# Optimization experiments

Hardware: AMD Instinct MI355X
Metric: run time of the kernel (lower is better)

Reference implementation:

```python
import jax, jax.numpy as jnp
import numpy as np

B, S, HID = 4, 2048, 2048
NH, NKV = 8, 1
HD = HID // NH  # 256
G = NH // NKV   # queries per kv head
ROPE_THETA = 10000.0
NEG_INF = -1e9


def setup_inputs() -> dict:
    key = jax.random.key(0)
    ks = jax.random.split(key, 4)
    x = jax.random.normal(ks[0], (B, S, HID), jnp.float32)
    qkv_dim = (NH + 2 * NKV) * HD
    w_qkv = jax.random.normal(ks[1], (HID, qkv_dim), jnp.float32) * (HID ** -0.5)
    b_qkv = jnp.zeros((qkv_dim,), jnp.float32)
    w_o = jax.random.normal(ks[2], (NH * HD, HID), jnp.float32) * ((NH * HD) ** -0.5)
    b_o = jnp.zeros((HID,), jnp.float32)
    # rotary table: cos/sin of position*inv_freq, interleaved-pair convention
    inv_freq = 1.0 / (ROPE_THETA ** (jnp.arange(0, HD, 2, dtype=jnp.float32) / HD))
    ang = jnp.outer(jnp.arange(S, dtype=jnp.float32), inv_freq)  # [S, HD/2]
    freqs_cis = jnp.stack([jnp.cos(ang), jnp.sin(ang)], axis=-1)  # [S, HD/2, 2]
    causal = jnp.tril(jnp.ones((S, S), bool))
    mask = jnp.where(causal, 0.0, NEG_INF).astype(jnp.float32)[None, None]  # [1,1,S,S]
    return dict(x=x, w_qkv=w_qkv, b_qkv=b_qkv, w_o=w_o, b_o=b_o,
                freqs_cis=freqs_cis, mask=mask)


def _rope(t, cos, sin):
    # t: [B,S,H,D]; cos/sin: [1,S,1,D/2]; interleaved complex pairs
    tp = t.reshape(*t.shape[:-1], -1, 2)
    r, i = tp[..., 0], tp[..., 1]
    out = jnp.stack([r * cos - i * sin, r * sin + i * cos], axis=-1)
    return out.reshape(t.shape)


def reference(x, w_qkv, b_qkv, w_o, b_o, freqs_cis, mask):
    b, s, _ = x.shape
    qkv = x @ w_qkv + b_qkv
    q, k, v = jnp.split(qkv, [NH * HD, NH * HD + NKV * HD], axis=-1)
    q = q.reshape(b, s, NH, HD)
    k = k.reshape(b, s, NKV, HD)
    v = v.reshape(b, s, NKV, HD)
    cos = freqs_cis[..., 0][None, :, None, :]
    sin = freqs_cis[..., 1][None, :, None, :]
    q = _rope(q, cos, sin)
    k = _rope(k, cos, sin)
    # GQA: head h attends with kv group h // G (same layout as repeat_interleave)
    qh = q.transpose(0, 2, 1, 3).reshape(b, NKV, G, s, HD)  # [B,KV,G,S,D]
    kh = k.transpose(0, 2, 1, 3)                            # [B,KV,S,D]
    vh = v.transpose(0, 2, 1, 3)
    scores = jnp.einsum('bkgqd,bksd->bkgqs', qh, kh) * (HD ** -0.5)
    scores = scores + mask[:, :, None]  # broadcast over group dim
    attn = jax.nn.softmax(scores.astype(jnp.float32), axis=-1).astype(q.dtype)
    out = jnp.einsum('bkgqs,bksd->bkgqd', attn, vh)         # [B,KV,G,S,D]
    out = out.reshape(b, NH, s, HD).transpose(0, 2, 1, 3).reshape(b, s, NH * HD)
    return out @ w_o + b_o
```

## Files before the change

kernel.cpp:

```cpp
#include <hip/hip_runtime.h>
#include <hip/hip_bf16.h>

#define B_ 4
#define S_ 2048
#define HID_ 2048
#define NH_ 8
#define HD_ 256
#define QKVN 2560

typedef unsigned short u16;
typedef unsigned long long ull;
typedef __attribute__((ext_vector_type(4))) float f32x4;
typedef __attribute__((ext_vector_type(16))) float f32x16;
typedef __attribute__((ext_vector_type(8))) short bf16x8;

__device__ __forceinline__ float bf2f(u16 u) {
  union { unsigned int i; float f; } v; v.i = ((unsigned int)u) << 16; return v.f;
}
__device__ __forceinline__ u16 f2bf(float f) {
  union { unsigned int i; float f; } v; v.f = f;
  unsigned int r = v.i + 0x7fffu + ((v.i >> 16) & 1u);
  return (u16)(r >> 16);
}

__global__ void cast_f32_bf16(const float* __restrict__ in, u16* __restrict__ out, int n8) {
  int i = blockIdx.x * blockDim.x + threadIdx.x;
  int stride = gridDim.x * blockDim.x;
  for (; i < n8; i += stride) {
    const float4* p = (const float4*)(in + (size_t)i * 8);
    float4 a = p[0], b = p[1];
    u16 o[8] = {f2bf(a.x), f2bf(a.y), f2bf(a.z), f2bf(a.w),
                f2bf(b.x), f2bf(b.y), f2bf(b.z), f2bf(b.w)};
    *(uint4*)(out + (size_t)i * 8) = *(const uint4*)o;
  }
}

__global__ void transpose_cast(const float* __restrict__ in, u16* __restrict__ out, int R, int C) {
  __shared__ float t[32][33];
  int c0 = blockIdx.x * 32, r0 = blockIdx.y * 32;
  int tx = threadIdx.x, ty = threadIdx.y;
#pragma unroll
  for (int i = 0; i < 4; ++i)
    t[ty + i * 8][tx] = in[(size_t)(r0 + ty + i * 8) * C + c0 + tx];
  __syncthreads();
#pragma unroll
  for (int i = 0; i < 4; ++i)
    out[(size_t)(c0 + ty + i * 8) * R + r0 + tx] = f2bf(t[tx][ty + i * 8]);
}

__global__ void transpose_bf16(const u16* __restrict__ in, u16* __restrict__ out, int R, int C) {
  __shared__ u16 t[32][33];
  in += (size_t)blockIdx.z * R * C;
  out += (size_t)blockIdx.z * R * C;
  int c0 = blockIdx.x * 32, r0 = blockIdx.y * 32;
  int tx = threadIdx.x, ty = threadIdx.y;
#pragma unroll
  for (int i = 0; i < 4; ++i)
    t[ty + i * 8][tx] = in[(size_t)(r0 + ty + i * 8) * C + c0 + tx];
  __syncthreads();
#pragma unroll
  for (int i = 0; i < 4; ++i)
    out[(size_t)(c0 + ty + i * 8) * R + r0 + tx] = t[tx][ty + i * 8];
}

template <bool OUT_F32>
__global__ __launch_bounds__(256) void gemm_bt(const u16* __restrict__ A, const u16* __restrict__ BT,
                                               const float* __restrict__ bias, void* __restrict__ Cout,
                                               int M, int N, int K) {
  __shared__ u16 As[128 * 32];
  __shared__ u16 Bs[128 * 32];
  int nwg = gridDim.x;
  int bid = (int)blockIdx.x;
  bid = (bid & 7) * (nwg >> 3) + (bid >> 3);
  int ntiles = N >> 7;
  int m0 = (bid / ntiles) << 7, n0 = (bid % ntiles) << 7;
  int tid = threadIdx.x, w = tid >> 6, lane = tid & 63;
  int wr = w >> 1, wc = w & 1;
  int l15 = lane & 15, lg = lane >> 4;
  f32x4 acc[4][4] = {};
  int crow = lane >> 2;
  int ccol = (lane & 3) * 8;
  for (int k0 = 0; k0 < K; k0 += 32) {
#pragma unroll
    for (int i = 0; i < 2; ++i) {
      int c = w * 2 + i;
      const u16* ga = A + (size_t)(m0 + c * 16 + crow) * K + k0 + ccol;
      const u16* gb = BT + (size_t)(n0 + c * 16 + crow) * K + k0 + ccol;
      __builtin_amdgcn_global_load_lds((const __attribute__((address_space(1))) void*)ga,
                                       (__attribute__((address_space(3))) void*)(As + c * 512), 16, 0, 0);
      __builtin_amdgcn_global_load_lds((const __attribute__((address_space(1))) void*)gb,
                                       (__attribute__((address_space(3))) void*)(Bs + c * 512), 16, 0, 0);
    }
    __syncthreads();
    bf16x8 af[4], bfr[4];
#pragma unroll
    for (int r = 0; r < 4; ++r)
      af[r] = *(const bf16x8*)&As[(wr * 64 + r * 16 + l15) * 32 + lg * 8];
#pragma unroll
    for (int c = 0; c < 4; ++c)
      bfr[c] = *(const bf16x8*)&Bs[(wc * 64 + c * 16 + l15) * 32 + lg * 8];
#pragma unroll
    for (int r = 0; r < 4; ++r)
#pragma unroll
      for (int c = 0; c < 4; ++c)
        acc[r][c] = __builtin_amdgcn_mfma_f32_16x16x32_bf16(af[r], bfr[c], acc[r][c], 0, 0, 0);
    __syncthreads();
  }
#pragma unroll
  for (int r = 0; r < 4; ++r) {
    int mrow = m0 + wr * 64 + r * 16 + lg * 4;
#pragma unroll
    for (int c = 0; c < 4; ++c) {
      int col = n0 + wc * 64 + c * 16 + l15;
      float bv = bias[col];
#pragma unroll
      for (int j = 0; j < 4; ++j) {
        float v = acc[r][c][j] + bv;
        if (OUT_F32)
          ((float*)Cout)[(size_t)(mrow + j) * N + col] = v;
        else
          ((u16*)Cout)[(size_t)(mrow + j) * N + col] = f2bf(v);
      }
    }
  }
}

__global__ void rope_scatter(const u16* __restrict__ qkv, const float* __restrict__ freqs,
                             u16* __restrict__ qo, u16* __restrict__ ko, u16* __restrict__ vo) {
  const int per_row = QKVN / 8;
  const int total = B_ * S_ * per_row;
  int i = blockIdx.x * blockDim.x + threadIdx.x;
  int stride = gridDim.x * blockDim.x;
  for (; i < total; i += stride) {
    int m = i / per_row;
    int n8 = (i - m * per_row) * 8;
    int b = m >> 11, s = m & 2047;
    uint4 raw = *(const uint4*)(qkv + (size_t)m * QKVN + n8);
    const u16* u = (const u16*)&raw;
    if (n8 < 2304) {
      int d = (n8 < 2048) ? (n8 & 255) : (n8 - 2048);
      float scl = (n8 < 2048) ? (0.0625f * 1.44269504f) : 1.0f;
      const float* fp = freqs + ((size_t)s * 128 + (d >> 1)) * 2;
      float4 f0 = *(const float4*)fp;
      float4 f1 = *(const float4*)(fp + 4);
      float fc[8] = {f0.x, f0.y, f0.z, f0.w, f1.x, f1.y, f1.z, f1.w};
      u16 o[8];
#pragma unroll
      for (int p = 0; p < 4; ++p) {
        float r = bf2f(u[2 * p]), im = bf2f(u[2 * p + 1]);
        float c = fc[2 * p], sn = fc[2 * p + 1];
        o[2 * p] = f2bf((r * c - im * sn) * scl);
        o[2 * p + 1] = f2bf((r * sn + im * c) * scl);
      }
      u16* dst;
      if (n8 < 2048) {
        dst = qo + (size_t)m * 2048 + n8;
      } else {
        dst = ko + (((size_t)m) << 8) + d;
      }
      *(uint4*)dst = *(const uint4*)o;
    } else {
      int d = n8 - 2304;
      *(uint4*)(vo + (((size_t)m) << 8) + d) = raw;
    }
  }
}

#define STAGE_K(bufofs, kt)                                                                       \
  do {                                                                                            \
    const u16* _src0 = Kp + ((size_t)(b * S_ + (kt) * 64)) * HD_;                                 \
    _Pragma("unroll") for (int _p = 0; _p < 4; ++_p) {                                            \
      int _idx = _p * 512 + tid;                                                                  \
      int _row = _idx >> 5, _c = _idx & 31;                                                       \
      int _scol = (((_c * 16) ^ ((_row & 7) << 4)) >> 1);                                         \
      __builtin_amdgcn_global_load_lds(                                                           \
          (const __attribute__((address_space(1))) void*)(_src0 + (size_t)_row * HD_ + _scol),    \
          (__attribute__((address_space(3))) void*)(KsBase + (bufofs) + _idx * 8), 16, 0, 0);     \
    }                                                                                             \
  } while (0)

#define STAGE_V(bufofs, kt)                                                                       \
  do {                                                                                            \
    const u16* _src1 = VTp + (size_t)b * HD_ * S_ + (kt) * 64;                                    \
    _Pragma("unroll") for (int _p = 0; _p < 4; ++_p) {                                            \
      int _idx = _p * 512 + tid;                                                                  \
      int _d = _idx >> 3, _c = _idx & 7;                                                          \
      int _scol = (((_c * 16) ^ ((_d & 7) << 4)) >> 1);                                           \
      __builtin_amdgcn_global_load_lds(                                                           \
          (const __attribute__((address_space(1))) void*)(_src1 + (size_t)_d * S_ + _scol),       \
          (__attribute__((address_space(3))) void*)(VsBase + (bufofs) + _idx * 8), 16, 0, 0);     \
    }                                                                                             \
  } while (0)

#define FLASH_SEG_BODY()                                                                          \
  STAGE_K(0, kb);                                                                                 \
  STAGE_V(0, kb);                                                                                 \
  __syncthreads();                                                                                \
  int cur = 0;                                                                                    \
  for (int kt = kb; kt < ke; ++kt) {                                                              \
    if (kt + 1 < ke) {                                                                            \
      STAGE_K((cur ^ 1) * 16384, kt + 1);                                                         \
      STAGE_V((cur ^ 1) * 16384, kt + 1);                                                         \
    }                                                                                             \
    const char* Kb = (const char*)KsBase + cur * 32768;                                           \
    const char* Vb = (const char*)VsBase + cur * 32768;                                           \
    _Pragma("unroll") for (int tau = 0; tau < 2; ++tau) {                                         \
      int k0 = kt * 64 + tau * 32;                                                                \
      if (k0 > t * 32 + 31) break;                                                                \
      f32x16 scv = {};                                                                            \
      __builtin_amdgcn_s_setprio(1);                                                              \
      _Pragma("unroll") for (int st = 0; st < 16; ++st) {                                         \
        int row = tau * 32 + l31;                                                                 \
        bf16x8 kf = *(const bf16x8*)(Kb + row * 512 + ((st * 32 + lh * 16) ^ ((row & 7) << 4)));  \
        scv = __builtin_amdgcn_mfma_f32_32x32x16_bf16(kf, qf[st], scv, 0, 0, 0);                  \
      }                                                                                           \
      __builtin_amdgcn_s_setprio(0);                                                              \
      if (k0 + 31 > t * 32) {                                                                     \
        _Pragma("unroll") for (int jj = 0; jj < 16; ++jj) {                                       \
          int kg = k0 + (jj & 3) + 8 * (jj >> 2) + 4 * lh;                                        \
          if (kg > s_g) scv[jj] = -3.0e38f;                                                       \
        }                                                                                         \
      }                                                                                           \
      float tmax = -3.0e38f;                                                                      \
      _Pragma("unroll") for (int jj = 0; jj < 16; ++jj) tmax = fmaxf(tmax, scv[jj]);              \
      tmax = fmaxf(tmax, __shfl_xor(tmax, 32));                                                   \
      if (!__all(tmax - m_r <= 8.0f)) {                                                           \
        float mnew = fmaxf(m_r, tmax);                                                            \
        float sc = exp2f(m_r - mnew);                                                             \
        l_r *= sc;                                                                                \
        _Pragma("unroll") for (int dt = 0; dt < 8; ++dt) oacc[dt] *= sc;                          \
        m_r = mnew;                                                                               \
      }                                                                                           \
      float ts = 0.f;                                                                             \
      unsigned cpk[8];                                                                            \
      _Pragma("unroll") for (int mi = 0; mi < 8; ++mi) {                                          \
        float p0 = exp2f(scv[2 * mi] - m_r);                                                      \
        float p1 = exp2f(scv[2 * mi + 1] - m_r);                                                  \
        ts += p0 + p1;                                                                            \
        cpk[mi] = ((unsigned)f2bf(p1) << 16) | f2bf(p0);                                          \
      }                                                                                           \
      ts += __shfl_xor(ts, 32);                                                                   \
      l_r += ts;                                                                                  \
      asm volatile("v_permlane32_swap_b32 %0, %1" : "+v"(cpk[0]), "+v"(cpk[2]));                  \
      asm volatile("v_permlane32_swap_b32 %0, %1" : "+v"(cpk[1]), "+v"(cpk[3]));                  \
      asm volatile("v_permlane32_swap_b32 %0, %1" : "+v"(cpk[4]), "+v"(cpk[6]));                  \
      asm volatile("v_permlane32_swap_b32 %0, %1" : "+v"(cpk[5]), "+v"(cpk[7]));                  \
      union { unsigned u[4]; bf16x8 v; } pa, pb;                                                  \
      pa.u[0] = cpk[0]; pa.u[1] = cpk[1]; pa.u[2] = cpk[2]; pa.u[3] = cpk[3];                     \
      pb.u[0] = cpk[4]; pb.u[1] = cpk[5]; pb.u[2] = cpk[6]; pb.u[3] = cpk[7];                     \
      __builtin_amdgcn_s_setprio(1);                                                              \
      _Pragma("unroll") for (int dt = 0; dt < 8; ++dt) {                                          \
        int d = dt * 32 + l31;                                                                    \
        int swz = (d & 7) << 4;                                                                   \
        bf16x8 va = *(const bf16x8*)(Vb + d * 128 + (((2 * tau) * 32 + lh * 16) ^ swz));          \
        oacc[dt] = __builtin_amdgcn_mfma_f32_32x32x16_bf16(va, pa.v, oacc[dt], 0, 0, 0);          \
        bf16x8 vb2 = *(const bf16x8*)(Vb + d * 128 + (((2 * tau + 1) * 32 + lh * 16) ^ swz));     \
        oacc[dt] = __builtin_amdgcn_mfma_f32_32x32x16_bf16(vb2, pb.v, oacc[dt], 0, 0, 0);         \
      }                                                                                           \
      __builtin_amdgcn_s_setprio(0);                                                              \
    }                                                                                             \
    __syncthreads();                                                                              \
    cur ^= 1;                                                                                     \
  }

__global__ __launch_bounds__(512, 2) void flash_attn(const u16* __restrict__ Qp, const u16* __restrict__ Kp,
                                                     const u16* __restrict__ VTp, u16* __restrict__ Op) {
  __shared__ u16 Ks[2][64 * 256];
  __shared__ u16 Vs[2][256 * 64];
  int bid = (int)blockIdx.x;
  int b = bid & 3, t = bid >> 2;
  int tid = threadIdx.x;
  int w = tid >> 6, l = tid & 63;
  int l31 = l & 31, lh = l >> 5;
  int q_local = w * 32 + l31;
  size_t qrow = (size_t)b * 16384 + (size_t)t * 256 + q_local;
  int s_g = t * 32 + (q_local >> 3);
  u16* KsBase = &Ks[0][0];
  u16* VsBase = &Vs[0][0];
  bf16x8 qf[16];
  const u16* qp = Qp + qrow * HD_ + lh * 8;
#pragma unroll
  for (int st = 0; st < 16; ++st) qf[st] = *(const bf16x8*)(qp + st * 16);
  f32x16 oacc[8] = {};
  float m_r = -3.0e38f, l_r = 0.f;
  int kb = 0, ke = t / 2 + 1;
  FLASH_SEG_BODY();
  float inv = 1.0f / l_r;
  u16* ob = Op + qrow * 256;
#pragma unroll
  for (int dt = 0; dt < 8; ++dt) {
#pragma unroll
    for (int jj = 0; jj < 4; ++jj) {
      int d0 = dt * 32 + jj * 8 + 4 * lh;
      u16 o4[4];
#pragma unroll
      for (int e = 0; e < 4; ++e) o4[e] = f2bf(oacc[dt][jj * 4 + e] * inv);
      *(ull*)(ob + d0) = *(const ull*)o4;
    }
  }
}

__global__ __launch_bounds__(512, 2) void flash_attn_split(const u16* __restrict__ Qp, const u16* __restrict__ Kp,
                                                           const u16* __restrict__ VTp, u16* __restrict__ P0,
                                                           float* __restrict__ ml0, float* __restrict__ ml1,
                                                           u16* __restrict__ Op) {
  __shared__ u16 Ks[2][64 * 256];
  __shared__ u16 Vs[2][256 * 64];
  int bid = (int)blockIdx.x;
  int b = (bid & 7) >> 1;
  int j = ((bid & 1) << 5) + (bid >> 3);
  int tid = threadIdx.x;
  int w = tid >> 6, l = tid & 63;
  int l31 = l & 31, lh = l >> 5;
  int q_local = w * 32 + l31;
  u16* KsBase = &Ks[0][0];
  u16* VsBase = &Vs[0][0];

  for (int seg = 0; seg < 2; ++seg) {
    int t = seg ? (63 - j) : j;
    int nkv = (t >> 1) + 1;
    int half = (nkv + 1) >> 1;
    int kb = seg ? half : 0;
    int ke = seg ? nkv : half;
    size_t qrow = (size_t)b * 16384 + (size_t)t * 256 + q_local;
    int s_g = t * 32 + (q_local >> 3);
    float* mlbuf = seg ? ml1 : ml0;
    if (kb >= ke) {
      if (lh == 0) { mlbuf[qrow * 2] = -3.0e38f; mlbuf[qrow * 2 + 1] = 0.f; }
      continue;
    }
    bf16x8 qf[16];
    const u16* qp = Qp + qrow * HD_ + lh * 8;
#pragma unroll
    for (int st = 0; st < 16; ++st) qf[st] = *(const bf16x8*)(qp + st * 16);
    f32x16 oacc[8] = {};
    float m_r = -3.0e38f, l_r = 0.f;
    FLASH_SEG_BODY();
    float inv = 1.0f / l_r;
    u16* ob = (seg ? Op : P0) + qrow * 256;
#pragma unroll
    for (int dt = 0; dt < 8; ++dt) {
#pragma unroll
      for (int jj = 0; jj < 4; ++jj) {
        int d0 = dt * 32 + jj * 8 + 4 * lh;
        u16 o4[4];
#pragma unroll
        for (int e = 0; e < 4; ++e) o4[e] = f2bf(oacc[dt][jj * 4 + e] * inv);
        *(ull*)(ob + d0) = *(const ull*)o4;
      }
    }
    if (lh == 0) { mlbuf[qrow * 2] = m_r; mlbuf[qrow * 2 + 1] = l_r; }
  }
}

__global__ __launch_bounds__(256) void combine_parts(const u16* __restrict__ P0, const float* __restrict__ ml0,
                                                     const float* __restrict__ ml1, u16* __restrict__ O) {
  int r = blockIdx.x * 256 + threadIdx.x;
  float m0 = ml0[(size_t)r * 2], l0 = ml0[(size_t)r * 2 + 1];
  float m1 = ml1[(size_t)r * 2], l1 = ml1[(size_t)r * 2 + 1];
  float M = fmaxf(m0, m1);
  float w0 = l0 * exp2f(m0 - M), w1 = l1 * exp2f(m1 - M);
  float inv = 1.0f / (w0 + w1);
  w0 *= inv; w1 *= inv;
  const u16* p0 = P0 + (size_t)r * 256;
  u16* p1 = O + (size_t)r * 256;
#pragma unroll 4
  for (int c = 0; c < 32; ++c) {
    uint4 a = *(const uint4*)(p0 + c * 8);
    uint4 bq = *(const uint4*)(p1 + c * 8);
    const u16* ua = (const u16*)&a;
    const u16* ub = (const u16*)&bq;
    u16 o[8];
#pragma unroll
    for (int e = 0; e < 8; ++e) o[e] = f2bf(w0 * bf2f(ua[e]) + w1 * bf2f(ub[e]));
    *(uint4*)(p1 + c * 8) = *(const uint4*)o;
  }
}

extern "C" void kernel_launch(void* const* d_in, const int* in_sizes, int n_in,
                              void* d_out, int out_size, void* d_ws, size_t ws_size,
                              hipStream_t stream) {
  const float* x = (const float*)d_in[0];
  const float* w_qkv = (const float*)d_in[1];
  const float* b_qkv = (const float*)d_in[2];
  const float* w_o = (const float*)d_in[3];
  const float* b_o = (const float*)d_in[4];
  const float* freqs = (const float*)d_in[5];

  char* ws = (char*)d_ws;
  u16* xb    = (u16*)ws;
  u16* wqkvT = (u16*)(ws + 33554432);
  u16* woT   = (u16*)(ws + 44040192);
  u16* qkv   = (u16*)(ws + 52428800);
  u16* qall  = (u16*)(ws + 94371840);
  u16* kbuf  = (u16*)(ws + 127926272);
  u16* vbuf  = (u16*)(ws + 132120576);
  u16* part0 = (u16*)(ws + 136314880);
  float* ml0 = (float*)(ws + 169869312);
  float* ml1 = (float*)(ws + 170393600);
  u16* vT    = xb;
  u16* attout = qkv;

  bool split = (ws_size >= 170917888ULL);

  cast_f32_bf16<<<2048, 256, 0, stream>>>(x, xb, (B_ * S_ * HID_) / 8);
  transpose_cast<<<dim3(QKVN / 32, HID_ / 32), dim3(32, 8), 0, stream>>>(w_qkv, wqkvT, HID_, QKVN);
  transpose_cast<<<dim3(HID_ / 32, HID_ / 32), dim3(32, 8), 0, stream>>>(w_o, woT, HID_, HID_);
  gemm_bt<false><<<dim3(64 * 20), 256, 0, stream>>>(xb, wqkvT, b_qkv, qkv, B_ * S_, QKVN, HID_);
  rope_scatter<<<2048, 256, 0, stream>>>(qkv, freqs, qall, kbuf, vbuf);
  transpose_bf16<<<dim3(HD_ / 32, S_ / 32, B_), dim3(32, 8), 0, stream>>>(vbuf, vT, S_, HD_);
  if (split) {
    flash_attn_split<<<256, 512, 0, stream>>>(qall, kbuf, vT, part0, ml0, ml1, attout);
    combine_parts<<<256, 256, 0, stream>>>(part0, ml0, ml1, attout);
  } else {
    flash_attn<<<256, 512, 0, stream>>>(qall, kbuf, vT, attout);
  }
  gemm_bt<true><<<dim3(64 * 16), 256, 0, stream>>>(attout, woT, b_o, d_out, B_ * S_, HID_, HID_);
}
```

Baseline: 483.1 us.

## Rework K/V LDS swizzle to remove bank conflicts and parallelize combine

Changes the XOR swizzle used when staging K and V tiles into LDS. K now uses a full 32-way chunk XOR by row, and V is repacked as 128x128 with two d-rows per LDS row and a 16-way XOR. The MFMA fragment reads are updated to match, which should cut LDS bank conflicts in the attention inner loops. The combine kernel now gives each thread one 16-byte chunk instead of a whole row, launching 8192 blocks for more memory parallelism. This adds some address arithmetic per load.

```diff
diff --git a/kernel.cpp b/kernel.cpp
--- a/kernel.cpp
+++ b/kernel.cpp
@@ -166,28 +166,30 @@
   }
 }
 
+
 #define STAGE_K(bufofs, kt)                                                                       \
   do {                                                                                            \
-    const u16* _src0 = Kp + ((size_t)(b * S_ + (kt) * 64)) * HD_;                                 \
     _Pragma("unroll") for (int _p = 0; _p < 4; ++_p) {                                            \
       int _idx = _p * 512 + tid;                                                                  \
       int _row = _idx >> 5, _c = _idx & 31;                                                       \
-      int _scol = (((_c * 16) ^ ((_row & 7) << 4)) >> 1);                                         \
+      const u16* _src = Kp + ((size_t)(b * S_ + (kt) * 64 + _row)) * HD_ +                        \
+                        ((_c ^ (_row & 31)) * 8);                                                 \
       __builtin_amdgcn_global_load_lds(                                                           \
-          (const __attribute__((address_space(1))) void*)(_src0 + (size_t)_row * HD_ + _scol),    \
+          (const __attribute__((address_space(1))) void*)_src,                                    \
           (__attribute__((address_space(3))) void*)(KsBase + (bufofs) + _idx * 8), 16, 0, 0);     \
     }                                                                                             \
   } while (0)
 
 #define STAGE_V(bufofs, kt)                                                                       \
   do {                                                                                            \
-    const u16* _src1 = VTp + (size_t)b * HD_ * S_ + (kt) * 64;                                    \
     _Pragma("unroll") for (int _p = 0; _p < 4; ++_p) {                                            \
       int _idx = _p * 512 + tid;                                                                  \
-      int _d = _idx >> 3, _c = _idx & 7;                                                          \
-      int _scol = (((_c * 16) ^ ((_d & 7) << 4)) >> 1);                                           \
+      int _r = _idx >> 4, _gp = _idx & 15;                                                        \
+      int _g = _gp ^ (_r & 15);                                                                   \
+      int _d = _r * 2 + (_g >> 3), _c = _g & 7;                                                   \
+      const u16* _src = VTp + ((size_t)(b * 256 + _d)) * S_ + (kt) * 64 + _c * 8;                 \
       __builtin_amdgcn_global_load_lds(                                                           \
-          (const __attribute__((address_space(1))) void*)(_src1 + (size_t)_d * S_ + _scol),       \
+          (const __attribute__((address_space(1))) void*)_src,                                    \
           (__attribute__((address_space(3))) void*)(VsBase + (bufofs) + _idx * 8), 16, 0, 0);     \
     }                                                                                             \
   } while (0)
@@ -202,16 +204,16 @@
       STAGE_K((cur ^ 1) * 16384, kt + 1);                                                         \
       STAGE_V((cur ^ 1) * 16384, kt + 1);                                                         \
     }                                                                                             \
-    const char* Kb = (const char*)KsBase + cur * 32768;                                           \
-    const char* Vb = (const char*)VsBase + cur * 32768;                                           \
+    const char* Kb = (const char*)(KsBase + cur * 16384);                                         \
+    const char* Vb = (const char*)(VsBase + cur * 16384);                                         \
     _Pragma("unroll") for (int tau = 0; tau < 2; ++tau) {                                         \
       int k0 = kt * 64 + tau * 32;                                                                \
       if (k0 > t * 32 + 31) break;                                                                \
+      int row = tau * 32 + l31;                                                                   \
       f32x16 scv = {};                                                                            \
       __builtin_amdgcn_s_setprio(1);                                                              \
       _Pragma("unroll") for (int st = 0; st < 16; ++st) {                                         \
-        int row = tau * 32 + l31;                                                                 \
-        bf16x8 kf = *(const bf16x8*)(Kb + row * 512 + ((st * 32 + lh * 16) ^ ((row & 7) << 4)));  \
+        bf16x8 kf = *(const bf16x8*)(Kb + row * 512 + (((st * 2 + lh) ^ l31) << 4));              \
         scv = __builtin_amdgcn_mfma_f32_32x32x16_bf16(kf, qf[st], scv, 0, 0, 0);                  \
       }                                                                                           \
       __builtin_amdgcn_s_setprio(0);                                                              \
@@ -251,10 +253,12 @@
       __builtin_amdgcn_s_setprio(1);                                                              \
       _Pragma("unroll") for (int dt = 0; dt < 8; ++dt) {                                          \
         int d = dt * 32 + l31;                                                                    \
-        int swz = (d & 7) << 4;                                                                   \
-        bf16x8 va = *(const bf16x8*)(Vb + d * 128 + (((2 * tau) * 32 + lh * 16) ^ swz));          \
+        int rr = d >> 1;                                                                          \
+        int gb = (d & 1) * 8 + tau * 4;                                                           \
+        int rx = (rr & 15) << 4;                                                                  \
+        bf16x8 va = *(const bf16x8*)(Vb + rr * 256 + (((gb + lh) << 4) ^ rx));                    \
         oacc[dt] = __builtin_amdgcn_mfma_f32_32x32x16_bf16(va, pa.v, oacc[dt], 0, 0, 0);          \
-        bf16x8 vb2 = *(const bf16x8*)(Vb + d * 128 + (((2 * tau + 1) * 32 + lh * 16) ^ swz));     \
+        bf16x8 vb2 = *(const bf16x8*)(Vb + rr * 256 + (((gb + 2 + lh) << 4) ^ rx));               \
         oacc[dt] = __builtin_amdgcn_mfma_f32_32x32x16_bf16(vb2, pb.v, oacc[dt], 0, 0, 0);         \
       }                                                                                           \
       __builtin_amdgcn_s_setprio(0);                                                              \
@@ -266,7 +270,7 @@
 __global__ __launch_bounds__(512, 2) void flash_attn(const u16* __restrict__ Qp, const u16* __restrict__ Kp,
                                                      const u16* __restrict__ VTp, u16* __restrict__ Op) {
   __shared__ u16 Ks[2][64 * 256];
-  __shared__ u16 Vs[2][256 * 64];
+  __shared__ u16 Vs[2][128 * 128];
   int bid = (int)blockIdx.x;
   int b = bid & 3, t = bid >> 2;
   int tid = threadIdx.x;
@@ -305,7 +309,7 @@
                                                            float* __restrict__ ml0, float* __restrict__ ml1,
                                                            u16* __restrict__ Op) {
   __shared__ u16 Ks[2][64 * 256];
-  __shared__ u16 Vs[2][256 * 64];
+  __shared__ u16 Vs[2][128 * 128];
   int bid = (int)blockIdx.x;
   int b = (bid & 7) >> 1;
   int j = ((bid & 1) << 5) + (bid >> 3);
@@ -355,26 +359,23 @@
 
 __global__ __launch_bounds__(256) void combine_parts(const u16* __restrict__ P0, const float* __restrict__ ml0,
                                                      const float* __restrict__ ml1, u16* __restrict__ O) {
-  int r = blockIdx.x * 256 + threadIdx.x;
+  int idx = blockIdx.x * 256 + threadIdx.x;
+  int r = idx >> 5;
+  int c = (idx & 31) * 8;
   float m0 = ml0[(size_t)r * 2], l0 = ml0[(size_t)r * 2 + 1];
   float m1 = ml1[(size_t)r * 2], l1 = ml1[(size_t)r * 2 + 1];
   float M = fmaxf(m0, m1);
   float w0 = l0 * exp2f(m0 - M), w1 = l1 * exp2f(m1 - M);
   float inv = 1.0f / (w0 + w1);
   w0 *= inv; w1 *= inv;
-  const u16* p0 = P0 + (size_t)r * 256;
-  u16* p1 = O + (size_t)r * 256;
-#pragma unroll 4
-  for (int c = 0; c < 32; ++c) {
-    uint4 a = *(const uint4*)(p0 + c * 8);
-    uint4 bq = *(const uint4*)(p1 + c * 8);
-    const u16* ua = (const u16*)&a;
-    const u16* ub = (const u16*)&bq;
-    u16 o[8];
-#pragma unroll
-    for (int e = 0; e < 8; ++e) o[e] = f2bf(w0 * bf2f(ua[e]) + w1 * bf2f(ub[e]));
-    *(uint4*)(p1 + c * 8) = *(const uint4*)o;
-  }
+  uint4 a = *(const uint4*)(P0 + (size_t)r * 256 + c);
+  uint4 bq = *(const uint4*)(O + (size_t)r * 256 + c);
+  const u16* ua = (const u16*)&a;
+  const u16* ub = (const u16*)&bq;
+  u16 o[8];
+#pragma unroll
+  for (int e = 0; e < 8; ++e) o[e] = f2bf(w0 * bf2f(ua[e]) + w1 * bf2f(ub[e]));
+  *(uint4*)(O + (size_t)r * 256 + c) = *(const uint4*)o;
 }
 
 extern "C" void kernel_launch(void* const* d_in, const int* in_sizes, int n_in,
@@ -411,7 +412,7 @@
   transpose_bf16<<<dim3(HD_ / 32, S_ / 32, B_), dim3(32, 8), 0, stream>>>(vbuf, vT, S_, HD_);
   if (split) {
     flash_attn_split<<<256, 512, 0, stream>>>(qall, kbuf, vT, part0, ml0, ml1, attout);
-    combine_parts<<<256, 256, 0, stream>>>(part0, ml0, ml1, attout);
+    combine_parts<<<8192, 256, 0, stream>>>(part0, ml0, ml1, attout);
   } else {
     flash_attn<<<256, 512, 0, stream>>>(qall, kbuf, vT, attout);
   }
```

Result: faster. 421.7 us (-12.7%).
